# Optimization experiments

Measured on AMD Instinct MI355X. Metric: run time of the kernel, lower is better.

The kernel has to match this reference:

```python
import jax, jax.numpy as jnp
import numpy as np

B, CIN, COUT, T = 64, 2048, 2048, 128
BLOCK = 8            # structured-sparsity block size from _create_structured_sparse_mask
SPARSITY = 0.9       # keep probability per block = 1 - SPARSITY
SPIKE_PROB = 0.1     # binary input spike rate


def setup_inputs() -> dict:
    key = jax.random.key(0)
    k1, k2, k3 = jax.random.split(key, 3)
    # binary input spikes [B, Cin, T] (torch casts to int8; values are 0/1)
    spikes = (jax.random.uniform(k1, (B, CIN, T)) < SPIKE_PROB).astype(jnp.float32)
    # int8 quantized weights held as float32 (values in [-127,127))
    weights = jax.random.randint(k2, (COUT, CIN), -127, 127).astype(jnp.float32)
    # block-structured sparse connectivity mask, block 8x8, keep prob 0.1
    keep = jax.random.uniform(k3, (COUT // BLOCK, CIN // BLOCK)) > SPARSITY
    mask = jnp.repeat(jnp.repeat(keep, BLOCK, axis=0), BLOCK, axis=1).astype(jnp.float32)
    scale_exp = jnp.zeros((COUT,), dtype=jnp.int32)  # weight_scale_exp init zeros
    return {"spikes": spikes, "weights": weights, "mask": mask,
            "scale_exp": scale_exp, "threshold_exp": 7}


def reference(spikes, weights, mask, scale_exp, threshold_exp):
    # spikes: [B, Cin, T]; weights/mask: [Cout, Cin]; scale_exp: [Cout]
    masked_w = weights * mask                              # [Cout, Cin]
    scale = jnp.exp2(scale_exp.astype(jnp.float32))        # 2**weight_scale_exp per channel
    thr = jnp.float32(2.0) ** threshold_exp                # 2**threshold_exp (=128)
    s_t = jnp.transpose(spikes, (2, 0, 1))                 # [T, B, Cin]
    acc0 = jnp.zeros((spikes.shape[0], weights.shape[0]), jnp.float32)

    def step(acc, st):
        # integrate: sparse-masked matmul + power-of-two per-channel scale
        acc = acc + (st @ masked_w.T) * scale              # [B, Cout]
        spk = (acc >= thr).astype(jnp.float32)             # fire
        acc = acc * (1.0 - spk)                            # reset fired neurons to 0
        return acc, spk

    _, out = jax.lax.scan(step, acc0, s_t)                 # out: [T, B, Cout]
    return jnp.transpose(out, (1, 2, 0))                   # [B, Cout, T]
```

## Files before the change

### kernel.cpp

```cpp
#include <hip/hip_runtime.h>

#define BB   64
#define CIN  2048
#define COUT 2048
#define TT   128

#define NPAIR 64
#define NWIN  4
#define SLOTW 32

typedef int i32x4 __attribute__((ext_vector_type(4)));

__device__ __forceinline__ void async16(char* lds_dst, const char* g_src) {
    __builtin_amdgcn_global_load_lds(
        (const __attribute__((address_space(1))) void*)g_src,
        (__attribute__((address_space(3))) void*)lds_dst,
        16, 0, 0);
}

__global__ void prep1(const float* __restrict__ spikes,
                      const float* __restrict__ msk,
                      char* __restrict__ A,
                      unsigned long long* __restrict__ kb) {
    int bid = blockIdx.x;
    int tid = threadIdx.x;

    if (bid >= 2048) {
        int rb = bid - 2048;
        bool keep = (msk[(size_t)(rb * 8) * CIN + tid * 8] != 0.f);
        unsigned long long m = __ballot(keep);
        if ((tid & 63) == 0) kb[rb * 4 + (tid >> 6)] = m;
        return;
    }

    __shared__ float tile[32][256];
    int cg = bid & 7, tg = (bid >> 3) & 3, b = bid >> 5;
    int c0 = cg * 256, t0 = tg * 32;

    {
        const float* src = spikes + ((size_t)b * CIN + c0 + tid) * TT + t0;
#pragma unroll
        for (int j = 0; j < 8; ++j) {
            float4 v = *(const float4*)(src + j * 4);
            tile[j * 4 + 0][tid] = v.x;
            tile[j * 4 + 1][tid] = v.y;
            tile[j * 4 + 2][tid] = v.z;
            tile[j * 4 + 3][tid] = v.w;
        }
    }
    __syncthreads();

    const int cq = tid & 63, tw = tid >> 6;
#pragma unroll
    for (int s2 = 0; s2 < 8; ++s2) {
        int t = s2 * 4 + tw;
        float4 v = *(const float4*)&tile[t][cq * 4];
        unsigned pk = (v.x != 0.f ? 0x1u : 0u) | (v.y != 0.f ? 0x100u : 0u) |
                      (v.z != 0.f ? 0x10000u : 0u) | (v.w != 0.f ? 0x1000000u : 0u);
        *(unsigned*)(A + ((size_t)(b * TT) + t0 + t) * CIN + c0 + cq * 4) = pk;
    }
}

__global__ void prep2(const float* __restrict__ w,
                      const float* __restrict__ msk,
                      const unsigned long long* __restrict__ kb,
                      char* __restrict__ Bc,
                      unsigned short* __restrict__ lst,
                      unsigned* __restrict__ ofs_g,
                      unsigned* __restrict__ nch_g) {
    __shared__ unsigned snch[256];
    __shared__ unsigned sofs[256];
    __shared__ unsigned sbm_self;
    __shared__ short skl[SLOTW];
    const int tid = threadIdx.x;
    const int pw_self = blockIdx.x;

    {
        int p = tid >> 2, wdw = tid & 3;
        unsigned long long r = kb[(4 * p + 0) * 4 + wdw] | kb[(4 * p + 1) * 4 + wdw] |
                               kb[(4 * p + 2) * 4 + wdw] | kb[(4 * p + 3) * 4 + wdw];
        unsigned long long t2 = r | (r >> 1);
        unsigned bm = 0u;
#pragma unroll
        for (int s = 0; s < 32; ++s)
            bm |= (unsigned)((t2 >> (2 * s)) & 1ull) << s;
        if (tid == pw_self) sbm_self = bm;
        snch[tid] = (unsigned)((__popc(bm) + 3) >> 2);
    }
    __syncthreads();
    if (tid == 0) {
        unsigned run = 0;
#pragma unroll 4
        for (int i = 0; i < 256; ++i) { sofs[i] = run; run += snch[i] * 4; }
        ofs_g[pw_self] = sofs[pw_self];
        nch_g[pw_self] = snch[pw_self];
        unsigned rem = sbm_self;
        unsigned ns = snch[pw_self] * 4;
        unsigned o0 = sofs[pw_self];
        for (unsigned j = 0; j < ns; ++j) {
            int kl = -1;
            if (rem) { kl = __ffs(rem) - 1; rem &= rem - 1u; }
            skl[j] = (short)kl;
            lst[o0 + j] = (unsigned short)(kl >= 0 ? kl : 0);
        }
    }
    __syncthreads();

    const int p = pw_self >> 2, wdw = pw_self & 3;
    const unsigned o = sofs[pw_self];
    const unsigned nslots = snch[pw_self] * 4;

    const int col = (tid & 127) >> 2, q = tid & 3;
    const unsigned jo = tid >> 7;
    for (unsigned j0 = 0; j0 < nslots; j0 += 2) {
        unsigned j = j0 + jo;
        if (j < nslots) {
            int kl = skl[j];
            unsigned pk = 0u;
            if (kl >= 0) {
                int kk = wdw * SLOTW + kl;
                size_t base = (size_t)(p * 32 + col) * CIN + kk * 16 + q * 4;
                float4 a = *(const float4*)(w + base);
                float4 m = *(const float4*)(msk + base);
                int b0 = (int)(char)(int)(a.x * m.x);
                int b1 = (int)(char)(int)(a.y * m.y);
                int b2 = (int)(char)(int)(a.z * m.z);
                int b3 = (int)(char)(int)(a.w * m.w);
                pk = (unsigned)((b0 & 0xFF) | ((b1 & 0xFF) << 8) | ((b2 & 0xFF) << 16) | (b3 << 24));
            }
            *(unsigned*)(Bc + (size_t)(o + j) * 512 + col * 16 + q * 4) = pk;
        }
    }
}

__global__ void __launch_bounds__(512, 2)
snn_gemm_scan(const char* __restrict__ A,
              const char* __restrict__ Bc,
              const unsigned short* __restrict__ lst,
              const unsigned* __restrict__ ofs,
              const unsigned* __restrict__ nchv,
              const int* __restrict__ scale_exp,
              const int* __restrict__ thr_exp,
              float* __restrict__ out) {
    __shared__ __align__(16) union {
        char a[2][128 * 512];
        float c[128 * 132];
    } lds;
    __shared__ unsigned short slist[8][NWIN][SLOTW];
    __shared__ unsigned smeta_ofs[32];
    __shared__ unsigned smeta_nch[32];
    __shared__ unsigned pb[128 * 4];

    const int tid  = threadIdx.x;
    const int lane = tid & 63;
    const int w    = tid >> 6;

    const int bid = blockIdx.x;
    const int b  = bid & 63;
    const int nt = bid >> 6;
    const int m0 = b * TT;
    const int p0 = nt * 8;

    const int mrow = lane & 15, kc = lane >> 4;

    if (tid < 64) {
        int i = tid & 31;
        unsigned g = (p0 + (i >> 2)) * 4 + (i & 3);
        if (tid < 32) smeta_ofs[i] = ofs[g];
        else          smeta_nch[i] = nchv[g];
    }
    {
        int pl = tid >> 6;
        int rest = tid & 63;
        int w2 = rest >> 4, e = (rest & 15) * 2;
        unsigned g = (p0 + pl) * 4 + w2;
        unsigned o = ofs[g];
        *(unsigned*)&slist[pl][w2][e] = *(const unsigned*)(lst + o + e);
    }

    i32x4 acc[8][2] = {};

    auto stage = [&](int wdw, int buf) {
#pragma unroll
        for (int i = 0; i < 8; ++i) {
            int f = i * 512 + tid;
            int row = f >> 5, g0 = f & 31;
            int src = (g0 & ~7) | ((g0 & 7) ^ (row & 7));
            async16((char*)lds.a[buf] + (size_t)f * 16,
                    A + (size_t)(m0 + row) * CIN + wdw * 512 + src * 16);
        }
    };

    stage(0, 0);
    stage(1, 1);
    asm volatile("s_waitcnt vmcnt(8) lgkmcnt(0)" ::: "memory");
    __builtin_amdgcn_s_barrier();

#pragma unroll
    for (int wdw = 0; wdw < NWIN; ++wdw) {
        const char* sa = (const char*)lds.a[wdw & 1];
        const unsigned o   = smeta_ofs[w * 4 + wdw];
        const unsigned nch = smeta_nch[w * 4 + wdw];
        const unsigned short* Lp = &slist[w][wdw][0];
        const char* bbase = Bc + (size_t)o * 512 + mrow * 16 + (size_t)kc * 512;

        if (nch) {
            int   kkN = (int)Lp[kc];
            i32x4 b0N = *(const i32x4*)bbase;
            i32x4 b1N = *(const i32x4*)(bbase + 256);
            for (unsigned c = 0; c < nch; ++c) {
                const int   kkC = kkN;
                const i32x4 b0C = b0N, b1C = b1N;
                if (c + 1 < nch) {
                    kkN = (int)Lp[(c + 1) * 4 + kc];
                    b0N = *(const i32x4*)(bbase + (size_t)(c + 1) * 2048);
                    b1N = *(const i32x4*)(bbase + (size_t)(c + 1) * 2048 + 256);
                }
                const int swz = mrow * 512 + ((kkC ^ (mrow & 7)) << 4);
                i32x4 av[8];
#pragma unroll
                for (int mf = 0; mf < 8; ++mf)
                    av[mf] = *(const i32x4*)(sa + mf * 8192 + swz);
#pragma unroll
                for (int mf = 0; mf < 8; ++mf) {
                    acc[mf][0] = __builtin_amdgcn_mfma_i32_16x16x64_i8(
                        av[mf], b0C, acc[mf][0], 0, 0, 0);
                    acc[mf][1] = __builtin_amdgcn_mfma_i32_16x16x64_i8(
                        av[mf], b1C, acc[mf][1], 0, 0, 0);
                }
            }
        }

        __builtin_amdgcn_s_barrier();
        if (wdw + 1 < NWIN) {
            if (wdw + 2 < NWIN) {
                stage(wdw + 2, wdw & 1);
                asm volatile("s_waitcnt vmcnt(8)" ::: "memory");
            } else {
                asm volatile("s_waitcnt vmcnt(0)" ::: "memory");
            }
            __builtin_amdgcn_s_barrier();
        }
    }

    const float thr = exp2f((float)thr_exp[0]);
#pragma unroll
    for (int P = 0; P < 2; ++P) {
        __syncthreads();
        if ((w >> 2) == P) {
            const int rb = (lane >> 4) * 4;
            const int cb = lane & 15;
            const int cbase = (w & 3) * 32;
#pragma unroll
            for (int mf = 0; mf < 8; ++mf)
#pragma unroll
                for (int cf = 0; cf < 2; ++cf)
#pragma unroll
                    for (int r = 0; r < 4; ++r)
                        lds.c[(mf * 16 + rb + r) * 132 + cbase + cf * 16 + cb] =
                            (float)acc[mf][cf][r];
        }
        __syncthreads();

        if (tid < 128) {
            const float scale = exp2f((float)scale_exp[nt * 256 + P * 128 + tid]);
            float a = 0.f;
#pragma unroll
            for (int q = 0; q < 4; ++q) {
                unsigned bq = 0u;
#pragma unroll 8
                for (int j = 0; j < 32; ++j) {
                    a += lds.c[(q * 32 + j) * 132 + tid] * scale;
                    unsigned sp = (a >= thr) ? 1u : 0u;
                    if (sp) a = 0.f;
                    bq |= sp << j;
                }
                pb[tid * 4 + q] = bq;
            }
        }
        __syncthreads();

        const int t4 = tid & 31, u = tid >> 5;
#pragma unroll
        for (int s2 = 0; s2 < 8; ++s2) {
            int co = s2 * 16 + u;
            unsigned wb  = pb[co * 4 + (t4 >> 3)];
            unsigned nib = (wb >> ((t4 & 7) * 4)) & 0xFu;
            float4 v;
            v.x = (float)(nib & 1u);
            v.y = (float)((nib >> 1) & 1u);
            v.z = (float)((nib >> 2) & 1u);
            v.w = (float)((nib >> 3) & 1u);
            *(float4*)(out + (size_t)(b * COUT + nt * 256 + P * 128 + co) * TT
                       + t4 * 4) = v;
        }
    }
}

extern "C" void kernel_launch(void* const* d_in, const int* in_sizes, int n_in,
                              void* d_out, int out_size, void* d_ws, size_t ws_size,
                              hipStream_t stream) {
    const float* spikes  = (const float*)d_in[0];
    const float* weights = (const float*)d_in[1];
    const float* mask    = (const float*)d_in[2];
    const int*   scale_e = (const int*)d_in[3];
    const int*   thr_e   = (const int*)d_in[4];
    float* out = (float*)d_out;

    char* ws = (char*)d_ws;
    char*               Ai8  = ws;
    char*               Bc   = ws + 16777216;
    unsigned short*     lstp = (unsigned short*)(ws + 20709376);
    unsigned*           ofsp = (unsigned*)(ws + 20725760);
    unsigned*           nchp = (unsigned*)(ws + 20726784);
    unsigned long long* kbp  = (unsigned long long*)(ws + 20727808);

    prep1<<<2048 + 256, 256, 0, stream>>>(spikes, mask, Ai8, kbp);
    prep2<<<NPAIR * NWIN, 256, 0, stream>>>(weights, mask, kbp, Bc, lstp, ofsp, nchp);
    snn_gemm_scan<<<8 * BB, 512, 0, stream>>>(Ai8, Bc, lstp, ofsp, nchp,
                                              scale_e, thr_e, out);
}
```

Measured before the change: 209.2 us.

## Halve K-window size, shrink LDS, and do the spike scan with in-register shuffles

```diff
diff --git a/kernel.cpp b/kernel.cpp
--- a/kernel.cpp
+++ b/kernel.cpp
@@ -6,8 +6,8 @@
 #define TT   128
 
 #define NPAIR 64
-#define NWIN  4
-#define SLOTW 32
+#define NWIN  8
+#define SLOTW 16
 
 typedef int i32x4 __attribute__((ext_vector_type(4)));
 
@@ -68,35 +68,55 @@
                       unsigned short* __restrict__ lst,
                       unsigned* __restrict__ ofs_g,
                       unsigned* __restrict__ nch_g) {
-    __shared__ unsigned snch[256];
-    __shared__ unsigned sofs[256];
-    __shared__ unsigned sbm_self;
+    __shared__ unsigned sbm[256];
+    __shared__ unsigned short snch[512];
+    __shared__ unsigned sofs[512];
+    __shared__ unsigned partial[64];
     __shared__ short skl[SLOTW];
     const int tid = threadIdx.x;
-    const int pw_self = blockIdx.x;
+    const int pw = blockIdx.x;
 
     {
-        int p = tid >> 2, wdw = tid & 3;
-        unsigned long long r = kb[(4 * p + 0) * 4 + wdw] | kb[(4 * p + 1) * 4 + wdw] |
-                               kb[(4 * p + 2) * 4 + wdw] | kb[(4 * p + 3) * 4 + wdw];
+        int p = tid >> 2, j = tid & 3;
+        unsigned long long r = kb[(4 * p + 0) * 4 + j] | kb[(4 * p + 1) * 4 + j] |
+                               kb[(4 * p + 2) * 4 + j] | kb[(4 * p + 3) * 4 + j];
         unsigned long long t2 = r | (r >> 1);
         unsigned bm = 0u;
 #pragma unroll
         for (int s = 0; s < 32; ++s)
             bm |= (unsigned)((t2 >> (2 * s)) & 1ull) << s;
-        if (tid == pw_self) sbm_self = bm;
-        snch[tid] = (unsigned)((__popc(bm) + 3) >> 2);
+        sbm[tid] = bm;
+    }
+    __syncthreads();
+    for (int e = tid; e < 512; e += 256) {
+        int p = e >> 3, wdw = e & 7;
+        unsigned bm16 = (sbm[p * 4 + (wdw >> 1)] >> ((wdw & 1) * 16)) & 0xFFFFu;
+        snch[e] = (unsigned short)((__popc(bm16) + 3) >> 2);
+    }
+    __syncthreads();
+    if (tid < 64) {
+        unsigned run = 0;
+        for (int k = 0; k < 8; ++k) run += (unsigned)snch[tid * 8 + k] * 4;
+        partial[tid] = run;
     }
     __syncthreads();
     if (tid == 0) {
         unsigned run = 0;
-#pragma unroll 4
-        for (int i = 0; i < 256; ++i) { sofs[i] = run; run += snch[i] * 4; }
-        ofs_g[pw_self] = sofs[pw_self];
-        nch_g[pw_self] = snch[pw_self];
-        unsigned rem = sbm_self;
-        unsigned ns = snch[pw_self] * 4;
-        unsigned o0 = sofs[pw_self];
+        for (int i = 0; i < 64; ++i) { unsigned t = partial[i]; partial[i] = run; run += t; }
+    }
+    __syncthreads();
+    if (tid < 64) {
+        unsigned run = partial[tid];
+        for (int k = 0; k < 8; ++k) { sofs[tid * 8 + k] = run; run += (unsigned)snch[tid * 8 + k] * 4; }
+    }
+    __syncthreads();
+    if (tid == 0) {
+        ofs_g[pw] = sofs[pw];
+        nch_g[pw] = snch[pw];
+        unsigned bm16 = (sbm[(pw >> 3) * 4 + ((pw & 7) >> 1)] >> (((pw & 7) & 1) * 16)) & 0xFFFFu;
+        unsigned rem = bm16;
+        unsigned ns = (unsigned)snch[pw] * 4;
+        unsigned o0 = sofs[pw];
         for (unsigned j = 0; j < ns; ++j) {
             int kl = -1;
             if (rem) { kl = __ffs(rem) - 1; rem &= rem - 1u; }
@@ -106,9 +126,9 @@
     }
     __syncthreads();
 
-    const int p = pw_self >> 2, wdw = pw_self & 3;
-    const unsigned o = sofs[pw_self];
-    const unsigned nslots = snch[pw_self] * 4;
+    const int p = pw >> 3, wdw = pw & 7;
+    const unsigned o = sofs[pw];
+    const unsigned nslots = (unsigned)snch[pw] * 4;
 
     const int col = (tid & 127) >> 2, q = tid & 3;
     const unsigned jo = tid >> 7;
@@ -133,7 +153,7 @@
     }
 }
 
-__global__ void __launch_bounds__(512, 2)
+__global__ void __launch_bounds__(512, 4)
 snn_gemm_scan(const char* __restrict__ A,
               const char* __restrict__ Bc,
               const unsigned short* __restrict__ lst,
@@ -142,14 +162,11 @@
               const int* __restrict__ scale_exp,
               const int* __restrict__ thr_exp,
               float* __restrict__ out) {
-    __shared__ __align__(16) union {
-        char a[2][128 * 512];
-        float c[128 * 132];
-    } lds;
+    __shared__ __align__(16) char lds_a[2][128 * 256];
     __shared__ unsigned short slist[8][NWIN][SLOTW];
-    __shared__ unsigned smeta_ofs[32];
-    __shared__ unsigned smeta_nch[32];
-    __shared__ unsigned pb[128 * 4];
+    __shared__ unsigned smeta_ofs[64];
+    __shared__ unsigned smeta_nch[64];
+    __shared__ unsigned pb[256 * 4];
 
     const int tid  = threadIdx.x;
     const int lane = tid & 63;
@@ -163,17 +180,17 @@
 
     const int mrow = lane & 15, kc = lane >> 4;
 
-    if (tid < 64) {
-        int i = tid & 31;
-        unsigned g = (p0 + (i >> 2)) * 4 + (i & 3);
-        if (tid < 32) smeta_ofs[i] = ofs[g];
+    if (tid < 128) {
+        int i = tid & 63;
+        unsigned g = (p0 + (i >> 3)) * 8 + (i & 7);
+        if (tid < 64) smeta_ofs[i] = ofs[g];
         else          smeta_nch[i] = nchv[g];
     }
     {
         int pl = tid >> 6;
         int rest = tid & 63;
-        int w2 = rest >> 4, e = (rest & 15) * 2;
-        unsigned g = (p0 + pl) * 4 + w2;
+        int w2 = rest >> 3, e = (rest & 7) * 2;
+        unsigned g = (p0 + pl) * 8 + w2;
         unsigned o = ofs[g];
         *(unsigned*)&slist[pl][w2][e] = *(const unsigned*)(lst + o + e);
     }
@@ -182,25 +199,25 @@
 
     auto stage = [&](int wdw, int buf) {
 #pragma unroll
-        for (int i = 0; i < 8; ++i) {
+        for (int i = 0; i < 4; ++i) {
             int f = i * 512 + tid;
-            int row = f >> 5, g0 = f & 31;
+            int row = f >> 4, g0 = f & 15;
             int src = (g0 & ~7) | ((g0 & 7) ^ (row & 7));
-            async16((char*)lds.a[buf] + (size_t)f * 16,
-                    A + (size_t)(m0 + row) * CIN + wdw * 512 + src * 16);
+            async16(lds_a[buf] + (size_t)f * 16,
+                    A + (size_t)(m0 + row) * CIN + wdw * 256 + src * 16);
         }
     };
 
     stage(0, 0);
     stage(1, 1);
-    asm volatile("s_waitcnt vmcnt(8) lgkmcnt(0)" ::: "memory");
+    asm volatile("s_waitcnt vmcnt(4) lgkmcnt(0)" ::: "memory");
     __builtin_amdgcn_s_barrier();
 
 #pragma unroll
     for (int wdw = 0; wdw < NWIN; ++wdw) {
-        const char* sa = (const char*)lds.a[wdw & 1];
-        const unsigned o   = smeta_ofs[w * 4 + wdw];
-        const unsigned nch = smeta_nch[w * 4 + wdw];
+        const char* sa = lds_a[wdw & 1];
+        const unsigned o   = smeta_ofs[w * 8 + wdw];
+        const unsigned nch = smeta_nch[w * 8 + wdw];
         const unsigned short* Lp = &slist[w][wdw][0];
         const char* bbase = Bc + (size_t)o * 512 + mrow * 16 + (size_t)kc * 512;
 
@@ -216,84 +233,85 @@
                     b0N = *(const i32x4*)(bbase + (size_t)(c + 1) * 2048);
                     b1N = *(const i32x4*)(bbase + (size_t)(c + 1) * 2048 + 256);
                 }
-                const int swz = mrow * 512 + ((kkC ^ (mrow & 7)) << 4);
-                i32x4 av[8];
-#pragma unroll
-                for (int mf = 0; mf < 8; ++mf)
-                    av[mf] = *(const i32x4*)(sa + mf * 8192 + swz);
-#pragma unroll
-                for (int mf = 0; mf < 8; ++mf) {
+                const int swz = mrow * 256 + ((kkC ^ (mrow & 7)) << 4);
+                i32x4 av[4];
+#pragma unroll
+                for (int mf = 0; mf < 4; ++mf)
+                    av[mf] = *(const i32x4*)(sa + mf * 4096 + swz);
+#pragma unroll
+                for (int mf = 0; mf < 4; ++mf) {
                     acc[mf][0] = __builtin_amdgcn_mfma_i32_16x16x64_i8(
                         av[mf], b0C, acc[mf][0], 0, 0, 0);
                     acc[mf][1] = __builtin_amdgcn_mfma_i32_16x16x64_i8(
                         av[mf], b1C, acc[mf][1], 0, 0, 0);
                 }
+#pragma unroll
+                for (int mf = 0; mf < 4; ++mf)
+                    av[mf] = *(const i32x4*)(sa + (4 + mf) * 4096 + swz);
+#pragma unroll
+                for (int mf = 0; mf < 4; ++mf) {
+                    acc[4 + mf][0] = __builtin_amdgcn_mfma_i32_16x16x64_i8(
+                        av[mf], b0C, acc[4 + mf][0], 0, 0, 0);
+                    acc[4 + mf][1] = __builtin_amdgcn_mfma_i32_16x16x64_i8(
+                        av[mf], b1C, acc[4 + mf][1], 0, 0, 0);
+                }
             }
         }
 
         __builtin_amdgcn_s_barrier();
-        if (wdw + 1 < NWIN) {
-            if (wdw + 2 < NWIN) {
-                stage(wdw + 2, wdw & 1);
-                asm volatile("s_waitcnt vmcnt(8)" ::: "memory");
-            } else {
-                asm volatile("s_waitcnt vmcnt(0)" ::: "memory");
+        if (wdw + 2 < NWIN) {
+            stage(wdw + 2, wdw & 1);
+            asm volatile("s_waitcnt vmcnt(4)" ::: "memory");
+            __builtin_amdgcn_s_barrier();
+        } else if (wdw + 1 < NWIN) {
+            asm volatile("s_waitcnt vmcnt(0)" ::: "memory");
+            __builtin_amdgcn_s_barrier();
+        }
+    }
+
+    const float thr = exp2f((float)thr_exp[0]);
+    const int ch = lane & 15;
+    const int grp = lane >> 4;
+    const float myscale = exp2f((float)scale_exp[nt * 256 + w * 32 + (grp & 1) * 16 + ch]);
+
+    float a = 0.f;
+    unsigned bq[4] = {0u, 0u, 0u, 0u};
+#pragma unroll
+    for (int mf = 0; mf < 8; ++mf)
+#pragma unroll
+        for (int hi = 0; hi < 4; ++hi) {
+            const int src = hi * 16 + ch;
+#pragma unroll
+            for (int r = 0; r < 4; ++r) {
+                int s0 = __shfl(acc[mf][0][r], src);
+                int s1 = __shfl(acc[mf][1][r], src);
+                float v = (float)((grp & 1) ? s1 : s0);
+                a = fmaf(v, myscale, a);
+                const int t = mf * 16 + hi * 4 + r;
+                unsigned sp = (a >= thr) ? 1u : 0u;
+                if (sp) a = 0.f;
+                bq[t >> 5] |= sp << (t & 31);
             }
-            __builtin_amdgcn_s_barrier();
-        }
-    }
-
-    const float thr = exp2f((float)thr_exp[0]);
-#pragma unroll
-    for (int P = 0; P < 2; ++P) {
-        __syncthreads();
-        if ((w >> 2) == P) {
-            const int rb = (lane >> 4) * 4;
-            const int cb = lane & 15;
-            const int cbase = (w & 3) * 32;
-#pragma unroll
-            for (int mf = 0; mf < 8; ++mf)
-#pragma unroll
-                for (int cf = 0; cf < 2; ++cf)
-#pragma unroll
-                    for (int r = 0; r < 4; ++r)
-                        lds.c[(mf * 16 + rb + r) * 132 + cbase + cf * 16 + cb] =
-                            (float)acc[mf][cf][r];
-        }
-        __syncthreads();
-
-        if (tid < 128) {
-            const float scale = exp2f((float)scale_exp[nt * 256 + P * 128 + tid]);
-            float a = 0.f;
-#pragma unroll
-            for (int q = 0; q < 4; ++q) {
-                unsigned bq = 0u;
-#pragma unroll 8
-                for (int j = 0; j < 32; ++j) {
-                    a += lds.c[(q * 32 + j) * 132 + tid] * scale;
-                    unsigned sp = (a >= thr) ? 1u : 0u;
-                    if (sp) a = 0.f;
-                    bq |= sp << j;
-                }
-                pb[tid * 4 + q] = bq;
-            }
-        }
-        __syncthreads();
-
-        const int t4 = tid & 31, u = tid >> 5;
-#pragma unroll
-        for (int s2 = 0; s2 < 8; ++s2) {
-            int co = s2 * 16 + u;
-            unsigned wb  = pb[co * 4 + (t4 >> 3)];
-            unsigned nib = (wb >> ((t4 & 7) * 4)) & 0xFu;
-            float4 v;
-            v.x = (float)(nib & 1u);
-            v.y = (float)((nib >> 1) & 1u);
-            v.z = (float)((nib >> 2) & 1u);
-            v.w = (float)((nib >> 3) & 1u);
-            *(float4*)(out + (size_t)(b * COUT + nt * 256 + P * 128 + co) * TT
-                       + t4 * 4) = v;
-        }
+        }
+    if (grp < 2) {
+        int cg = w * 32 + grp * 16 + ch;
+#pragma unroll
+        for (int q = 0; q < 4; ++q) pb[cg * 4 + q] = bq[q];
+    }
+    __syncthreads();
+
+    const int t4 = tid & 31, u = tid >> 5;
+#pragma unroll
+    for (int s2 = 0; s2 < 16; ++s2) {
+        int co = s2 * 16 + u;
+        unsigned wb  = pb[co * 4 + (t4 >> 3)];
+        unsigned nib = (wb >> ((t4 & 7) * 4)) & 0xFu;
+        float4 v;
+        v.x = (float)(nib & 1u);
+        v.y = (float)((nib >> 1) & 1u);
+        v.z = (float)((nib >> 2) & 1u);
+        v.w = (float)((nib >> 3) & 1u);
+        *(float4*)(out + (size_t)(b * COUT + nt * 256 + co) * TT + t4 * 4) = v;
     }
 }
 
@@ -310,10 +328,10 @@
     char* ws = (char*)d_ws;
     char*               Ai8  = ws;
     char*               Bc   = ws + 16777216;
-    unsigned short*     lstp = (unsigned short*)(ws + 20709376);
-    unsigned*           ofsp = (unsigned*)(ws + 20725760);
-    unsigned*           nchp = (unsigned*)(ws + 20726784);
-    unsigned long long* kbp  = (unsigned long long*)(ws + 20727808);
+    unsigned short*     lstp = (unsigned short*)(ws + 20973568);
+    unsigned*           ofsp = (unsigned*)(ws + 20990016);
+    unsigned*           nchp = (unsigned*)(ws + 20992064);
+    unsigned long long* kbp  = (unsigned long long*)(ws + 20994112);
 
     prep1<<<2048 + 256, 256, 0, stream>>>(spikes, mask, Ai8, kbp);
     prep2<<<NPAIR * NWIN, 256, 0, stream>>>(weights, mask, kbp, Bc, lstp, ofsp, nchp);
```

Result: slower. 244.5 us (+16.9%).
